# Optimization experiments

Hardware: AMD Instinct MI355X
Metric: run time of the kernel (lower is better)

The kernel has to match this reference:

```python
import jax, jax.numpy as jnp
import numpy as np

CHANNELS = 2048
MAX_ATOMS = 512
RNN_LAYERS = 4
LP_LAYERS = 3


def setup_inputs() -> dict:
    key = jax.random.key(0)
    ks = jax.random.split(key, 10)
    C = CHANNELS
    s = 1.0 / np.sqrt(C)  # pytorch default uniform init bound
    u = lambda k, shape: jax.random.uniform(k, shape, jnp.float32, -s, s)
    return {
        "x": jax.random.normal(ks[0], (1, C), jnp.float32),
        # LengthProducer: 3 hidden Linear(C,C)+LeakyReLU(0.2), final Linear(C,1)
        "lp_w": u(ks[1], (LP_LAYERS, C, C)),
        "lp_b": u(ks[2], (LP_LAYERS, C)),
        "lp_wout": u(ks[3], (1, C)),
        "lp_bout": u(ks[4], (1,)),
        # nn.RNN(C, C, 4, nonlinearity='relu') parameters
        "w_ih": u(ks[5], (RNN_LAYERS, C, C)),
        "b_ih": u(ks[6], (RNN_LAYERS, C)),
        "w_hh": u(ks[7], (RNN_LAYERS, C, C)),
        "b_hh": u(ks[8], (RNN_LAYERS, C)),
        "max_atoms": MAX_ATOMS,
    }


def _unit_norm(t):
    # torch: x / (norm(x, dim=1, keepdim=True) + 1e-12); axis 1 has size 1 here
    n = jnp.linalg.norm(t, axis=1, keepdims=True)
    return t / (n + 1e-12)


def reference(x, lp_w, lp_b, lp_wout, lp_bout, w_ih, b_ih, w_hh, b_hh, max_atoms):
    C = x.shape[-1]
    x = x.reshape(1, C)

    # ---- LengthProducer: l = clamp(|MLP(x)|, 0, 0.9999) ----
    y = x
    for i in range(LP_LAYERS):
        y = jax.nn.leaky_relu(y @ lp_w[i].T + lp_b[i], 0.2)
    l = jnp.clip(jnp.abs(y @ lp_wout.T + lp_bout), 0.0, 0.9999)  # (1,1)

    # ---- 4-layer ReLU RNN scan with per-step unit-norm ----
    inp0 = jnp.zeros((1, 1, C), x.dtype)
    hid0 = jnp.zeros((RNN_LAYERS, 1, C), x.dtype).at[0].set(x)

    def step(carry, _):
        inp, hid = carry  # (1,1,C), (L,1,C)
        h_in = inp[0]  # (1,C)
        new_h = []
        for layer in range(RNN_LAYERS):
            h = jax.nn.relu(h_in @ w_ih[layer].T + b_ih[layer]
                            + hid[layer] @ w_hh[layer].T + b_hh[layer])
            new_h.append(h)
            h_in = h
        inp = _unit_norm(h_in[None])          # (1,1,C)
        hid = _unit_norm(jnp.stack(new_h))     # (L,1,C)
        return (inp, hid), inp[0, 0]           # emit (C,)

    _, seq = jax.lax.scan(step, (inp0, hid0), None, length=max_atoms)
    return seq, l  # seq: (max_atoms, C); original truncates to first int(l*max_atoms)+1 rows
```

## Files before the change

### kernel.cpp

```cpp
#include <hip/hip_runtime.h>


#define C      2048
#define NB     256
#define NT     512
#define STEPS  512

typedef unsigned long long u64;
typedef unsigned int u32;

#define F_INP   0
#define F_HIDB  (2*C)
#define F_HRAW  (10*C)

__device__ __forceinline__ float wred(float v) {
#pragma unroll
  for (int off = 32; off > 0; off >>= 1) v += __shfl_down(v, off, 64);
  return v;
}

__device__ __forceinline__ u64 pack(float val, int tag) {
  return ((u64)(unsigned)tag << 32) | (u64)__float_as_uint(val);
}
__device__ __forceinline__ void pub64(u64* p, float val, int tag) {
  __hip_atomic_store(p, pack(val, tag), __ATOMIC_RELAXED, __HIP_MEMORY_SCOPE_AGENT);
}
__device__ __forceinline__ u64 peek(u64* p) {
  return __hip_atomic_load(p, __ATOMIC_RELAXED, __HIP_MEMORY_SCOPE_AGENT);
}
__device__ __forceinline__ float val_of(u64 v) { return __uint_as_float((unsigned)v); }
__device__ __forceinline__ int   tag_of(u64 v) { return (int)(v >> 32); }

__device__ __forceinline__ float4 ldx4_dev(const float* p) {
  float4 r;
  asm volatile("global_load_dwordx4 %0, %1, off sc1\n\t"
               "s_waitcnt vmcnt(0)"
               : "=v"(r) : "v"(p) : "memory");
  return r;
}
__device__ __forceinline__ uint4 ldu4_dev(const u32* p) {
  uint4 r;
  asm volatile("global_load_dwordx4 %0, %1, off sc1\n\t"
               "s_waitcnt vmcnt(0)"
               : "=v"(r) : "v"(p) : "memory");
  return r;
}
__device__ __forceinline__ void stf_dev(float* p, float v) {
  __hip_atomic_store(p, v, __ATOMIC_RELAXED, __HIP_MEMORY_SCOPE_AGENT);
}

__device__ __forceinline__ void poll1(u64* __restrict__ A, int tagA,
                                      float* __restrict__ sa, int tid) {
  u64* a = A + 4 * tid;
  u64 va0, va1, va2, va3;
  for (;;) {
    va0 = peek(a + 0); va1 = peek(a + 1); va2 = peek(a + 2); va3 = peek(a + 3);
    bool ok = (tag_of(va0) == tagA) & (tag_of(va1) == tagA)
            & (tag_of(va2) == tagA) & (tag_of(va3) == tagA);
    if (ok) break;
    __builtin_amdgcn_s_sleep(2);
  }
  float4 fa = { val_of(va0), val_of(va1), val_of(va2), val_of(va3) };
  ((float4*)sa)[tid] = fa;
}

__global__ void init_kernel(const float* __restrict__ x, u64* __restrict__ ws) {
  float* f    = (float*)(ws + 3 * C);
  u32*   done = (u32*)(f + 13 * C);
  int i = blockIdx.x * blockDim.x + threadIdx.x;
  if (i < C) {
    f[F_INP + i]          = 0.f;
    f[F_HIDB + 0 * C + i] = x[i];
    f[F_HIDB + 1 * C + i] = 0.f;
    f[F_HIDB + 2 * C + i] = 0.f;
    f[F_HIDB + 3 * C + i] = 0.f;
  }
  if (i < NB) done[i] = 0;
}

__global__ __launch_bounds__(NT, 2) void rnn_persist(
    const float* __restrict__ x,
    const float* __restrict__ lp_w,  const float* __restrict__ lp_b,
    const float* __restrict__ lp_wout, const float* __restrict__ lp_bout,
    const float* __restrict__ w_ih,  const float* __restrict__ b_ih,
    const float* __restrict__ w_hh,  const float* __restrict__ b_hh,
    float* __restrict__ out, u64* __restrict__ ws)
{
  extern __shared__ float4 w3[];
  __shared__ __align__(16) float sh_a[C];
  __shared__ __align__(16) float sh_b[C];

  u64*   lp   = ws;
  float* f    = (float*)(ws + 3 * C);
  float* inp  = f + F_INP;
  float* hidb = f + F_HIDB;
  float* hraw = f + F_HRAW;
  u32*   done = (u32*)(f + 13 * C);

  const int tid  = threadIdx.x;
  const int lane = tid & 63;
  const int wid  = tid >> 6;
  const int j    = blockIdx.x * 8 + wid;

  const float4* WI = (const float4*)w_ih;
  const float4* WH = (const float4*)w_hh;
  float4 wir[3][8], whr[3][8];
#pragma unroll
  for (int l = 0; l < 3; ++l) {
    const size_t bi = (size_t)(l * C + j) * 512;
#pragma unroll
    for (int r = 0; r < 8; ++r) {
      wir[l][r] = WI[bi + r * 64 + lane];
      whr[l][r] = WH[bi + r * 64 + lane];
    }
  }
  {
    const size_t b3 = (size_t)(3 * C + j) * 512;
#pragma unroll
    for (int r = 0; r < 8; ++r) {
      w3[(wid * 2 + 0) * 512 + r * 64 + lane] = WI[b3 + r * 64 + lane];
      w3[(wid * 2 + 1) * 512 + r * 64 + lane] = WH[b3 + r * 64 + lane];
    }
  }
  float bias[4];
#pragma unroll
  for (int l = 0; l < 4; ++l) bias[l] = b_ih[l * C + j] + b_hh[l * C + j];
  __syncthreads();

  for (int s = 0; s < 3; ++s) {
    if (s == 0) ((float4*)sh_a)[tid] = ((const float4*)x)[tid];
    else        poll1(lp + (size_t)(s - 1) * C, s, sh_a, tid);
    __syncthreads();
    const float4* Wr  = (const float4*)(lp_w + ((size_t)s * C + j) * C);
    const float4* sa4 = (const float4*)sh_a;
    float a0 = 0, a1 = 0, a2 = 0, a3 = 0;
#pragma unroll
    for (int r = 0; r < 8; ++r) {
      float4 w = Wr[r * 64 + lane]; float4 h = sa4[r * 64 + lane];
      a0 = fmaf(w.x, h.x, a0); a1 = fmaf(w.y, h.y, a1);
      a2 = fmaf(w.z, h.z, a2); a3 = fmaf(w.w, h.w, a3);
    }
    float acc = wred((a0 + a1) + (a2 + a3));
    if (lane == 0) {
      float v = acc + lp_b[s * C + j];
      pub64(&lp[(size_t)s * C + j], (v >= 0.f) ? v : 0.2f * v, s + 1);
    }
    __syncthreads();
  }

  if (blockIdx.x == 0 && wid == 0) {
    float p = 0.f;
#pragma unroll
    for (int g = 0; g < 4; ++g) {
      u64 v[8];
      for (;;) {
        bool ok = true;
#pragma unroll
        for (int r = 0; r < 8; ++r)
          v[r] = peek(&lp[2 * C + (g * 8 + r) * 64 + lane]);
#pragma unroll
        for (int r = 0; r < 8; ++r) ok &= (tag_of(v[r]) == 3);
        if (ok) break;
        __builtin_amdgcn_s_sleep(2);
      }
#pragma unroll
      for (int r = 0; r < 8; ++r)
        p = fmaf(lp_wout[(g * 8 + r) * 64 + lane], val_of(v[r]), p);
    }
    p = wred(p);
    if (lane == 0) {
      float l = fabsf(p + lp_bout[0]);
      out[(size_t)STEPS * C] = fminf(l, 0.9999f);
    }
  }

  const int q = (tid + 2 * blockIdx.x) & (NT - 1);

  for (int t = 0; t < STEPS; ++t) {
    const int p = t & 1;
#pragma unroll
    for (int l = 0; l < 4; ++l) {
      const u32 tgt = (u32)(4 * t + l);

      const float* B = hidb + (size_t)(p * 4 + l) * C;
      float4 vb = ldx4_dev(B + 4 * q);
      ((float4*)sh_b)[q] = vb;

      if (tid < 64) {
        for (;;) {
          uint4 v = ldu4_dev(done + 4 * tid);
          bool ok = (v.x >= tgt) & (v.y >= tgt) & (v.z >= tgt) & (v.w >= tgt);
          if (__all(ok)) break;
          __builtin_amdgcn_s_sleep(2);
        }
      }
      __syncthreads();

      const float* A = (l == 0) ? (inp + (size_t)p * C)
                                : (hraw + (size_t)(l - 1) * C);
      float4 va = ldx4_dev(A + 4 * q);
      ((float4*)sh_a)[q] = va;
      __syncthreads();

      const float4* sa4 = (const float4*)sh_a;
      const float4* sb4 = (const float4*)sh_b;
      float a0 = 0, a1 = 0, a2 = 0, a3 = 0;
      if (l < 3) {
#pragma unroll
        for (int r = 0; r < 8; ++r) {
          float4 h = sa4[r * 64 + lane]; float4 w = wir[l][r];
          a0 = fmaf(w.x, h.x, a0); a1 = fmaf(w.y, h.y, a1);
          a2 = fmaf(w.z, h.z, a2); a3 = fmaf(w.w, h.w, a3);
          float4 g = sb4[r * 64 + lane]; float4 v = whr[l][r];
          a0 = fmaf(v.x, g.x, a0); a1 = fmaf(v.y, g.y, a1);
          a2 = fmaf(v.z, g.z, a2); a3 = fmaf(v.w, g.w, a3);
        }
      } else {
#pragma unroll
        for (int r = 0; r < 8; ++r) {
          float4 h = sa4[r * 64 + lane]; float4 w = w3[(wid * 2 + 0) * 512 + r * 64 + lane];
          a0 = fmaf(w.x, h.x, a0); a1 = fmaf(w.y, h.y, a1);
          a2 = fmaf(w.z, h.z, a2); a3 = fmaf(w.w, h.w, a3);
          float4 g = sb4[r * 64 + lane]; float4 v = w3[(wid * 2 + 1) * 512 + r * 64 + lane];
          a0 = fmaf(v.x, g.x, a0); a1 = fmaf(v.y, g.y, a1);
          a2 = fmaf(v.z, g.z, a2); a3 = fmaf(v.w, g.w, a3);
        }
      }
      float acc = wred((a0 + a1) + (a2 + a3));

      if (lane == 0) {
        float pre = acc + bias[l];
        float h   = fmaxf(pre, 0.f);
        float bin = h / (h + 1e-12f);
        if (l < 3) {
          stf_dev(&hraw[(size_t)l * C + j], h);
          stf_dev(&hidb[(size_t)((p ^ 1) * 4 + l) * C + j], bin);
        } else {
          stf_dev(&inp[(size_t)(p ^ 1) * C + j], bin);
          stf_dev(&hidb[(size_t)((p ^ 1) * 4 + 3) * C + j], bin);
          out[(size_t)t * C + j] = bin;
        }
      }
      __syncthreads();
      if (tid == 0)
        __hip_atomic_store(&done[blockIdx.x], tgt + 1,
                           __ATOMIC_RELAXED, __HIP_MEMORY_SCOPE_AGENT);
    }
  }
}

extern "C" void kernel_launch(void* const* d_in, const int* in_sizes, int n_in,
                              void* d_out, int out_size, void* d_ws, size_t ws_size,
                              hipStream_t stream) {
  const float* x       = (const float*)d_in[0];
  const float* lp_w    = (const float*)d_in[1];
  const float* lp_b    = (const float*)d_in[2];
  const float* lp_wout = (const float*)d_in[3];
  const float* lp_bout = (const float*)d_in[4];
  const float* w_ih    = (const float*)d_in[5];
  const float* b_ih    = (const float*)d_in[6];
  const float* w_hh    = (const float*)d_in[7];
  const float* b_hh    = (const float*)d_in[8];
  float* out = (float*)d_out;
  u64*   ws  = (u64*)d_ws;

  hipLaunchKernelGGL(init_kernel, dim3(8), dim3(256), 0, stream, x, ws);
  hipLaunchKernelGGL(rnn_persist, dim3(NB), dim3(NT),
                     8 * 2 * 512 * sizeof(float4) , stream,
                     x, lp_w, lp_b, lp_wout, lp_bout,
                     w_ih, b_ih, w_hh, b_hh, out, ws);
}
```

Baseline: 9.583 ms.

## Keep per-block normalized hidden states in LDS and cut global traffic per layer

Each block now recomputes the normalized hidden vectors (h/(h+eps)) locally from the single raw-h global buffer and keeps all four layers' normalized states in shared memory. This removes the separate global hidden-state reload and its extra store per layer step. Layer-3 weights move from dynamic LDS into registers, so all four layers use the same register path. The cost is higher register pressure (64 float4 of weights per thread) and redundant division work in every block, and ping-ponging a two-slot raw buffer relies on the done-counter barrier to prevent overwrite races.

```diff
diff --git a/kernel.cpp b/kernel.cpp
--- a/kernel.cpp
+++ b/kernel.cpp
@@ -8,10 +8,9 @@
 
 typedef unsigned long long u64;
 typedef unsigned int u32;
-
-#define F_INP   0
-#define F_HIDB  (2*C)
-#define F_HRAW  (10*C)
+typedef float vf4 __attribute__((ext_vector_type(4)));
+typedef unsigned int vu4 __attribute__((ext_vector_type(4)));
+
 
 __device__ __forceinline__ float wred(float v) {
 #pragma unroll
@@ -31,18 +30,18 @@
 __device__ __forceinline__ float val_of(u64 v) { return __uint_as_float((unsigned)v); }
 __device__ __forceinline__ int   tag_of(u64 v) { return (int)(v >> 32); }
 
-__device__ __forceinline__ float4 ldx4_dev(const float* p) {
-  float4 r;
+__device__ __forceinline__ vu4 ldu4_sc1(const u32* p) {
+  vu4 r;
   asm volatile("global_load_dwordx4 %0, %1, off sc1\n\t"
                "s_waitcnt vmcnt(0)"
-               : "=v"(r) : "v"(p) : "memory");
+               : "=&v"(r) : "v"(p) : "memory");
   return r;
 }
-__device__ __forceinline__ uint4 ldu4_dev(const u32* p) {
-  uint4 r;
+__device__ __forceinline__ vf4 ldf4_sc1(const float* p) {
+  vf4 r;
   asm volatile("global_load_dwordx4 %0, %1, off sc1\n\t"
                "s_waitcnt vmcnt(0)"
-               : "=v"(r) : "v"(p) : "memory");
+               : "=&v"(r) : "v"(p) : "memory");
   return r;
 }
 __device__ __forceinline__ void stf_dev(float* p, float v) {
@@ -64,17 +63,12 @@
   ((float4*)sa)[tid] = fa;
 }
 
-__global__ void init_kernel(const float* __restrict__ x, u64* __restrict__ ws) {
-  float* f    = (float*)(ws + 3 * C);
-  u32*   done = (u32*)(f + 13 * C);
+__global__ void init_kernel(u64* __restrict__ ws) {
+  u64*   lp   = ws;
+  float* hbuf = (float*)(ws + 3 * C);
+  u32*   done = (u32*)(hbuf + 2 * C);
   int i = blockIdx.x * blockDim.x + threadIdx.x;
-  if (i < C) {
-    f[F_INP + i]          = 0.f;
-    f[F_HIDB + 0 * C + i] = x[i];
-    f[F_HIDB + 1 * C + i] = 0.f;
-    f[F_HIDB + 2 * C + i] = 0.f;
-    f[F_HIDB + 3 * C + i] = 0.f;
-  }
+  if (i < C) { lp[i] = 0; lp[C + i] = 0; lp[2 * C + i] = 0; }
   if (i < NB) done[i] = 0;
 }
 
@@ -86,16 +80,12 @@
     const float* __restrict__ w_hh,  const float* __restrict__ b_hh,
     float* __restrict__ out, u64* __restrict__ ws)
 {
-  extern __shared__ float4 w3[];
   __shared__ __align__(16) float sh_a[C];
-  __shared__ __align__(16) float sh_b[C];
-
-  u64*   lp   = ws;
-  float* f    = (float*)(ws + 3 * C);
-  float* inp  = f + F_INP;
-  float* hidb = f + F_HIDB;
-  float* hraw = f + F_HRAW;
-  u32*   done = (u32*)(f + 13 * C);
+  __shared__ __align__(16) float bins[4][C];
+
+  u64*   lp    = ws;
+  float* hbuf  = (float*)(ws + 3 * C);
+  u32*   done_ = (u32*)(hbuf + 2 * C);
 
   const int tid  = threadIdx.x;
   const int lane = tid & 63;
@@ -104,9 +94,9 @@
 
   const float4* WI = (const float4*)w_ih;
   const float4* WH = (const float4*)w_hh;
-  float4 wir[3][8], whr[3][8];
-#pragma unroll
-  for (int l = 0; l < 3; ++l) {
+  float4 wir[4][8], whr[4][8];
+#pragma unroll
+  for (int l = 0; l < 4; ++l) {
     const size_t bi = (size_t)(l * C + j) * 512;
 #pragma unroll
     for (int r = 0; r < 8; ++r) {
@@ -114,18 +104,9 @@
       whr[l][r] = WH[bi + r * 64 + lane];
     }
   }
-  {
-    const size_t b3 = (size_t)(3 * C + j) * 512;
-#pragma unroll
-    for (int r = 0; r < 8; ++r) {
-      w3[(wid * 2 + 0) * 512 + r * 64 + lane] = WI[b3 + r * 64 + lane];
-      w3[(wid * 2 + 1) * 512 + r * 64 + lane] = WH[b3 + r * 64 + lane];
-    }
-  }
   float bias[4];
 #pragma unroll
   for (int l = 0; l < 4; ++l) bias[l] = b_ih[l * C + j] + b_hh[l * C + j];
-  __syncthreads();
 
   for (int s = 0; s < 3; ++s) {
     if (s == 0) ((float4*)sh_a)[tid] = ((const float4*)x)[tid];
@@ -174,76 +155,68 @@
     }
   }
 
+  {
+    vf4 z = {0.f, 0.f, 0.f, 0.f};
+    ((vf4*)bins[0])[tid] = z;
+    ((vf4*)bins[2])[tid] = z;
+    ((vf4*)bins[3])[tid] = z;
+    ((vf4*)bins[1])[tid] = ((const vf4*)x)[tid];
+  }
+
   const int q = (tid + 2 * blockIdx.x) & (NT - 1);
 
   for (int t = 0; t < STEPS; ++t) {
-    const int p = t & 1;
 #pragma unroll
     for (int l = 0; l < 4; ++l) {
-      const u32 tgt = (u32)(4 * t + l);
-
-      const float* B = hidb + (size_t)(p * 4 + l) * C;
-      float4 vb = ldx4_dev(B + 4 * q);
-      ((float4*)sh_b)[q] = vb;
-
-      if (tid < 64) {
-        for (;;) {
-          uint4 v = ldu4_dev(done + 4 * tid);
-          bool ok = (v.x >= tgt) & (v.y >= tgt) & (v.z >= tgt) & (v.w >= tgt);
-          if (__all(ok)) break;
-          __builtin_amdgcn_s_sleep(2);
+      const int s = 4 * t + l;
+
+      if (l > 0 || t > 0) {
+        if (tid < 64) {
+          for (;;) {
+            vu4 v = ldu4_sc1(done_ + 4 * lane);
+            bool ok = (v.x >= (u32)s) & (v.y >= (u32)s)
+                    & (v.z >= (u32)s) & (v.w >= (u32)s);
+            if (__all(ok)) break;
+            __builtin_amdgcn_s_sleep(2);
+          }
         }
+        __syncthreads();
+        const int hs = (l == 0) ? 1 : ((l - 1) & 1);
+        vf4 va = ldf4_sc1(hbuf + (size_t)hs * C + 4 * q);
+        ((vf4*)sh_a)[q] = va;
+        vf4 vb;
+        vb.x = va.x / (va.x + 1e-12f);
+        vb.y = va.y / (va.y + 1e-12f);
+        vb.z = va.z / (va.z + 1e-12f);
+        vb.w = va.w / (va.w + 1e-12f);
+        ((vf4*)bins[l])[q] = vb;
       }
       __syncthreads();
 
-      const float* A = (l == 0) ? (inp + (size_t)p * C)
-                                : (hraw + (size_t)(l - 1) * C);
-      float4 va = ldx4_dev(A + 4 * q);
-      ((float4*)sh_a)[q] = va;
-      __syncthreads();
-
-      const float4* sa4 = (const float4*)sh_a;
-      const float4* sb4 = (const float4*)sh_b;
+      const float4* sa4 = (l == 0) ? (const float4*)bins[0]
+                                   : (const float4*)sh_a;
+      const float4* sb4 = (const float4*)bins[(l + 1) & 3];
       float a0 = 0, a1 = 0, a2 = 0, a3 = 0;
-      if (l < 3) {
-#pragma unroll
-        for (int r = 0; r < 8; ++r) {
-          float4 h = sa4[r * 64 + lane]; float4 w = wir[l][r];
-          a0 = fmaf(w.x, h.x, a0); a1 = fmaf(w.y, h.y, a1);
-          a2 = fmaf(w.z, h.z, a2); a3 = fmaf(w.w, h.w, a3);
-          float4 g = sb4[r * 64 + lane]; float4 v = whr[l][r];
-          a0 = fmaf(v.x, g.x, a0); a1 = fmaf(v.y, g.y, a1);
-          a2 = fmaf(v.z, g.z, a2); a3 = fmaf(v.w, g.w, a3);
-        }
-      } else {
-#pragma unroll
-        for (int r = 0; r < 8; ++r) {
-          float4 h = sa4[r * 64 + lane]; float4 w = w3[(wid * 2 + 0) * 512 + r * 64 + lane];
-          a0 = fmaf(w.x, h.x, a0); a1 = fmaf(w.y, h.y, a1);
-          a2 = fmaf(w.z, h.z, a2); a3 = fmaf(w.w, h.w, a3);
-          float4 g = sb4[r * 64 + lane]; float4 v = w3[(wid * 2 + 1) * 512 + r * 64 + lane];
-          a0 = fmaf(v.x, g.x, a0); a1 = fmaf(v.y, g.y, a1);
-          a2 = fmaf(v.z, g.z, a2); a3 = fmaf(v.w, g.w, a3);
-        }
+#pragma unroll
+      for (int r = 0; r < 8; ++r) {
+        float4 h = sa4[r * 64 + lane]; float4 w = wir[l][r];
+        a0 = fmaf(w.x, h.x, a0); a1 = fmaf(w.y, h.y, a1);
+        a2 = fmaf(w.z, h.z, a2); a3 = fmaf(w.w, h.w, a3);
+        float4 g = sb4[r * 64 + lane]; float4 v = whr[l][r];
+        a0 = fmaf(v.x, g.x, a0); a1 = fmaf(v.y, g.y, a1);
+        a2 = fmaf(v.z, g.z, a2); a3 = fmaf(v.w, g.w, a3);
       }
       float acc = wred((a0 + a1) + (a2 + a3));
 
       if (lane == 0) {
         float pre = acc + bias[l];
         float h   = fmaxf(pre, 0.f);
-        float bin = h / (h + 1e-12f);
-        if (l < 3) {
-          stf_dev(&hraw[(size_t)l * C + j], h);
-          stf_dev(&hidb[(size_t)((p ^ 1) * 4 + l) * C + j], bin);
-        } else {
-          stf_dev(&inp[(size_t)(p ^ 1) * C + j], bin);
-          stf_dev(&hidb[(size_t)((p ^ 1) * 4 + 3) * C + j], bin);
-          out[(size_t)t * C + j] = bin;
-        }
+        stf_dev(&hbuf[(size_t)(l & 1) * C + j], h);
+        if (l == 3) out[(size_t)t * C + j] = h / (h + 1e-12f);
       }
       __syncthreads();
       if (tid == 0)
-        __hip_atomic_store(&done[blockIdx.x], tgt + 1,
+        __hip_atomic_store(&done_[blockIdx.x], (u32)(s + 1),
                            __ATOMIC_RELAXED, __HIP_MEMORY_SCOPE_AGENT);
     }
   }
@@ -264,9 +237,8 @@
   float* out = (float*)d_out;
   u64*   ws  = (u64*)d_ws;
 
-  hipLaunchKernelGGL(init_kernel, dim3(8), dim3(256), 0, stream, x, ws);
-  hipLaunchKernelGGL(rnn_persist, dim3(NB), dim3(NT),
-                     8 * 2 * 512 * sizeof(float4) , stream,
+  hipLaunchKernelGGL(init_kernel, dim3(8), dim3(256), 0, stream, ws);
+  hipLaunchKernelGGL(rnn_persist, dim3(NB), dim3(NT), 0, stream,
                      x, lp_w, lp_b, lp_wout, lp_bout,
                      w_ih, b_ih, w_hh, b_hh, out, ws);
 }
```

Result: slower. 13.47 ms (+40.5%).
